# Performance work log

Measured on AMD Instinct MI355X. Metric: run time of the kernel, lower is better.

The kernel has to match this reference:

```python
import jax, jax.numpy as jnp
import numpy as np
from functools import partial

C = 10   # number of regular-repr fields
G = 4    # C4 rotation group order
EPS = 1e-5


def _lift_kernel(w):
    """Lifting (trivial->regular) P4 kernel. w: [C, Cin, k, k] ->
    full kernel [C*G, Cin, k, k] with output channel layout (field, orientation)."""
    ks = [jnp.rot90(w, r, axes=(-2, -1)) for r in range(G)]  # each [C,Cin,k,k]
    k = jnp.stack(ks, axis=1)                                 # [C,G,Cin,k,k]
    return k.reshape(w.shape[0] * G, w.shape[1], w.shape[2], w.shape[3])


def _gconv_kernel(w):
    """Regular->regular P4 kernel. w: [Cout, Cin, G, k, k] (indexed by relative
    input orientation) -> full kernel [Cout*G, Cin*G, k, k].
    K[co*G+r, ci*G+s] = rot90(w[co, ci, (s-r) mod G], r)."""
    Cout, Cin, _, k1, k2 = w.shape
    ks = []
    for r in range(G):
        wr = jnp.roll(w, shift=r, axis=2)             # wr[..., s, :, :] = w[..., (s-r)%G]
        wr = jnp.rot90(wr, r, axes=(-2, -1))          # rotate spatially by r*90deg
        ks.append(wr)
    k = jnp.stack(ks, axis=1)                          # [Cout, G, Cin, G, k, k]
    return k.reshape(Cout * G, Cin * G, k1, k2)


def _conv(x, k, pad):
    return jax.lax.conv_general_dilated(
        x, k, window_strides=(1, 1), padding=pad,
        dimension_numbers=('NCHW', 'OIHW', 'NCHW'))


def _bn_relu(x, gamma, beta):
    """InnerBatchNorm (stats shared over the G orientations of each field) + ReLU."""
    B, CG, H, W = x.shape
    xr = x.reshape(B, C, G, H, W)
    m = xr.mean(axis=(0, 2, 3, 4), keepdims=True)
    v = xr.var(axis=(0, 2, 3, 4), keepdims=True)
    g = gamma[None, :, None, None, None]
    b = beta[None, :, None, None, None]
    y = (xr - m) * jax.lax.rsqrt(v + EPS) * g + b
    return jnp.maximum(y.reshape(B, CG, H, W), 0.0)


def _maxpool2(x):
    return jax.lax.reduce_window(x, -jnp.inf, jax.lax.max,
                                 (1, 1, 2, 2), (1, 1, 2, 2), 'VALID')


def setup_inputs() -> dict:
    key = jax.random.key(0)
    ks = jax.random.split(key, 20)
    B = 1024
    x = jax.random.normal(ks[0], (B, 1, 28, 28), dtype=jnp.float32)
    w1 = jax.random.normal(ks[1], (C, 1, 3, 3), dtype=jnp.float32) * 0.3
    w2 = jax.random.normal(ks[2], (C, C, G, 3, 3), dtype=jnp.float32) * 0.1
    w3 = jax.random.normal(ks[3], (C, C, G, 3, 3), dtype=jnp.float32) * 0.1
    w4 = jax.random.normal(ks[4], (C, C, G, 3, 3), dtype=jnp.float32) * 0.1
    w5 = jax.random.normal(ks[5], (C, C, G, 3, 3), dtype=jnp.float32) * 0.1
    w6 = jax.random.normal(ks[6], (C, C, G, 3, 3), dtype=jnp.float32) * 0.1
    w7 = jax.random.normal(ks[7], (C, C, G, 4, 4), dtype=jnp.float32) * 0.1
    g1 = jnp.ones((C,), jnp.float32) + 0.1 * jax.random.normal(ks[8], (C,))
    b1 = 0.1 * jax.random.normal(ks[9], (C,))
    g2 = jnp.ones((C,), jnp.float32) + 0.1 * jax.random.normal(ks[10], (C,))
    b2 = 0.1 * jax.random.normal(ks[11], (C,))
    gs = jnp.ones((C,), jnp.float32) + 0.1 * jax.random.normal(ks[12], (C,))
    bs = 0.1 * jax.random.normal(ks[13], (C,))
    wfc = jax.random.normal(ks[14], (10, C * 11 * 11), dtype=jnp.float32) * 0.05
    bfc = jnp.zeros((10,), jnp.float32)
    return dict(x=x, w1=w1, w2=w2, w3=w3, w4=w4, w5=w5, w6=w6, w7=w7,
                g1=g1, b1=b1, g2=g2, b2=b2, gs=gs, bs=bs, wfc=wfc, bfc=bfc)


PAD1 = [(1, 1), (1, 1)]
PAD0 = [(0, 0), (0, 0)]


def reference(x, w1, w2, w3, w4, w5, w6, w7, g1, b1, g2, b2, gs, bs, wfc, bfc):
    # block1: lifting P4 conv 3x3 pad1 + InnerBN + ReLU  -> [B, 40, 28, 28]
    h = _bn_relu(_conv(x, _lift_kernel(w1), PAD1), g1, b1)
    # block2: P4 conv + BN + ReLU + 2x2 max pool         -> [B, 40, 14, 14]
    h = _maxpool2(_bn_relu(_conv(h, _gconv_kernel(w2), PAD1), g2, b2))
    # blocks 3-6: P4 conv + shared BN/ReLU               -> [B, 40, 14, 14]
    for w in (w3, w4, w5, w6):
        h = _bn_relu(_conv(h, _gconv_kernel(w), PAD1), gs, bs)
    # block7: P4 conv 4x4 pad0 + shared BN/ReLU          -> [B, 40, 11, 11]
    h = _bn_relu(_conv(h, _gconv_kernel(w7), PAD0), gs, bs)
    # group pooling: max over the G orientations of each field -> [B, 10, 11, 11]
    B = h.shape[0]
    h = h.reshape(B, C, G, 11, 11).max(axis=2)
    # fc
    return h.reshape(B, -1) @ wfc.T + bfc
```

## Files before the change

### kernel.cpp

```cpp
#include <hip/hip_runtime.h>

#define EPSV 1e-5f
#define INV28 (1.f / 3211264.f)
#define INV14 (1.f / 802816.f)
#define INV11 (1.f / 495616.f)

typedef __bf16 v8bf __attribute__((ext_vector_type(8)));
typedef __bf16 v4bf __attribute__((ext_vector_type(4)));
typedef _Float16 v8h __attribute__((ext_vector_type(8)));
typedef _Float16 v4h __attribute__((ext_vector_type(4)));
typedef float v4f __attribute__((ext_vector_type(4)));

__device__ __forceinline__ int rotsrc(int r, int dy, int dx, int K) {
  int sy, sx;
  if (r == 0)      { sy = dy;       sx = dx; }
  else if (r == 1) { sy = dx;       sx = K - 1 - dy; }
  else if (r == 2) { sy = K - 1 - dy; sx = K - 1 - dx; }
  else             { sy = K - 1 - dx; sx = dy; }
  return sy * K + sx;
}

__device__ __forceinline__ float gw_val(const float* __restrict__ w, int oc, int g,
                                        int j, int KS) {
  int tap = g / 5, cig = g % 5, ci = cig * 8 + j;
  int co = oc >> 2, r = oc & 3, cin = ci >> 2, s = ci & 3;
  int srel = (s - r) & 3;
  return w[((co * 10 + cin) * 4 + srel) * (KS * KS) + rotsrc(r, tap / KS, tap % KS, KS)];
}

__device__ __forceinline__ float stat8a(const float* __restrict__ p, int i) {
  float v = 0.f;
#pragma unroll
  for (int c = 0; c < 8; ++c)
    v += __hip_atomic_load(&p[c * 32 + i], __ATOMIC_RELAXED, __HIP_MEMORY_SCOPE_AGENT);
  return v;
}

__global__ void prep_kernel(const float* __restrict__ w1, const float* __restrict__ w2,
                            const float* __restrict__ w3, const float* __restrict__ w4,
                            const float* __restrict__ w5, const float* __restrict__ w6,
                            const float* __restrict__ w7,
                            __bf16* __restrict__ K1b, __bf16* __restrict__ Wb,
                            float* __restrict__ stats) {
  int idx = blockIdx.x * blockDim.x + threadIdx.x;
  if (idx < 1792) { stats[idx] = 0.f; return; }
  idx -= 1792;
  if (idx < 1536) {
    int mt = idx >> 9, l = (idx >> 3) & 63, j = idx & 7;
    int m = l & 15, quad = l >> 4;
    int k = quad * 8 + j, oc = mt * 16 + m;
    float val = 0.f;
    if (k < 9 && oc < 40) {
      int c = oc >> 2, r = oc & 3;
      val = w1[c * 9 + rotsrc(r, k / 3, k % 3, 3)];
    }
    K1b[idx] = (__bf16)val;
    return;
  }
  idx -= 1536;
  if (idx < 92160) {
    int l = idx / 18432, r0 = idx % 18432;
    const float* w = (l == 0) ? w2 : (l == 1) ? w3 : (l == 2) ? w4 : (l == 3) ? w5 : w6;
    int mt = r0 / 6144, r1 = r0 % 6144;
    int c = r1 / 512, r2 = r1 % 512;
    int q = r2 / 128, r3 = r2 % 128;
    int ocl = r3 / 8, j = r3 % 8;
    int oc = mt * 16 + ocl, g = c * 4 + q;
    float val = 0.f;
    if (oc < 40 && g < 45) val = gw_val(w, oc, g, j, 3);
    Wb[idx] = (__bf16)val;
    return;
  }
  idx -= 92160;
  if (idx < 30720) {
    int mt = idx / 10240, r1 = idx % 10240;
    int c = r1 / 512, r2 = r1 % 512;
    int q = r2 / 128, r3 = r2 % 128;
    int ocl = r3 / 8, j = r3 % 8;
    int oc = mt * 16 + ocl, g = c * 4 + q;
    float val = 0.f;
    if (oc < 40) val = gw_val(w7, oc, g, j, 4);
    Wb[92160 + idx] = (__bf16)val;
  }
}

__global__ __launch_bounds__(256) void conv1_stats(
    const float* __restrict__ x, const __bf16* __restrict__ K1b,
    float* __restrict__ stats) {
  __shared__ float ximg[900];
  __shared__ float sstat[20];
  const int tid = threadIdx.x, img = blockIdx.x;
  if (tid < 20) sstat[tid] = 0.f;
  for (int i = tid; i < 900; i += 256) {
    int gy = i / 30 - 1, gx = i % 30 - 1;
    ximg[i] = (gy >= 0 && gy < 28 && gx >= 0 && gx < 28)
                  ? x[img * 784 + gy * 28 + gx] : 0.f;
  }
  __syncthreads();
  const int lane = tid & 63, wv = tid >> 6;
  const int m = lane & 15, quad = lane >> 4;
  v8bf a1[3];
#pragma unroll
  for (int mt = 0; mt < 3; ++mt)
    a1[mt] = *(const v8bf*)(K1b + (mt * 64 + lane) * 8);
  float s[3] = {0.f, 0.f, 0.f}, q[3] = {0.f, 0.f, 0.f};
  for (int st = wv; st < 49; st += 4) {
    const int p = st * 16 + m;
    const int y = p / 28, xx = p % 28;
    v8bf b;
#pragma unroll
    for (int j = 0; j < 8; ++j) {
      const int t = quad * 8 + j;
      float v = 0.f;
      if (t < 9) v = ximg[(y + t / 3) * 30 + xx + t % 3];
      b[j] = (__bf16)v;
    }
#pragma unroll
    for (int mt = 0; mt < 3; ++mt) {
      v4f acc = {0.f, 0.f, 0.f, 0.f};
      acc = __builtin_amdgcn_mfma_f32_16x16x32_bf16(a1[mt], b, acc, 0, 0, 0);
#pragma unroll
      for (int r = 0; r < 4; ++r) { float v = acc[r]; s[mt] += v; q[mt] += v * v; }
    }
  }
#pragma unroll
  for (int mt = 0; mt < 3; ++mt) {
    float sv = s[mt], qv = q[mt];
#pragma unroll
    for (int off = 1; off <= 8; off <<= 1) {
      sv += __shfl_xor(sv, off, 64);
      qv += __shfl_xor(qv, off, 64);
    }
    if (m == 0 && ((mt < 2) || (quad < 2))) {
      atomicAdd(&sstat[mt * 4 + quad], sv);
      atomicAdd(&sstat[10 + mt * 4 + quad], qv);
    }
  }
  __syncthreads();
  if (tid < 20) atomicAdd(&stats[(img & 7) * 32 + tid], sstat[tid]);
}

template<int R>
__global__ __launch_bounds__(256) void conv_band_fused(
    const float* __restrict__ x, const __bf16* __restrict__ K1b,
    const __bf16* __restrict__ Wl, const float* __restrict__ pstats,
    const float* __restrict__ pgamma, const float* __restrict__ pbeta,
    float pinvn, _Float16* __restrict__ T0, float* __restrict__ stats) {
  constexpr int NPIX = R * 28, NSUB = NPIX / 16, NSW = (NSUB + 3) / 4;
  constexpr int SROWS = R + 2, XR = R + 4;
  __shared__ __attribute__((aligned(16))) __bf16 tile[SROWS * 30 * 40];
  __shared__ float xpatch[XR * 32];
  __shared__ float sc[10], sh[10], sstat[20];
  const int tid = threadIdx.x;
  const int lane = tid & 63, wv = tid >> 6;
  const int m = lane & 15, quad = lane >> 4;
  int img, y0;
  if constexpr (R == 8) { img = blockIdx.x / 3; y0 = (blockIdx.x % 3) * 8; }
  else { img = blockIdx.x; y0 = 24; }

  if (tid < 20) sstat[tid] = 0.f;
  if (tid >= 32 && tid < 42) {
    int f = tid - 32;
    float mu = stat8a(pstats, f) * pinvn, q = stat8a(pstats, 10 + f) * pinvn;
    float isd = rsqrtf(q - mu * mu + EPSV);
    float s = pgamma[f] * isd;
    sc[f] = s; sh[f] = pbeta[f] - mu * s;
  }
  for (int i = tid; i < XR * 32; i += 256) {
    int gy = y0 - 2 + i / 32, gx = i % 32 - 2;
    xpatch[i] = (gy >= 0 && gy < 28 && gx >= 0 && gx < 28)
                    ? x[(long)img * 784 + gy * 28 + gx] : 0.f;
  }
  __syncthreads();

  {
    v8bf a1[3];
#pragma unroll
    for (int mt = 0; mt < 3; ++mt)
      a1[mt] = *(const v8bf*)(K1b + (mt * 64 + lane) * 8);
    constexpr int NPIXS = SROWS * 30;
    constexpr int NST = (NPIXS + 15) / 16;
    for (int st = wv; st < NST; st += 4) {
      const int p = st * 16 + m;
      const int pc = p < NPIXS ? p : NPIXS - 1;
      const int iy = pc / 30, ix = pc % 30;
      v8bf b;
#pragma unroll
      for (int j = 0; j < 8; ++j) {
        const int t = quad * 8 + j;
        float v = 0.f;
        if (t < 9) v = xpatch[(iy + t / 3) * 32 + ix + t % 3];
        b[j] = (__bf16)v;
      }
      const int gy = y0 + iy - 1, gx = ix - 1;
      const bool wr = p < NPIXS;
      const bool inb = wr && gy >= 0 && gy < 28 && gx >= 0 && gx < 28;
      __bf16* tb = &tile[pc * 40];
#pragma unroll
      for (int mt = 0; mt < 3; ++mt) {
        v4f acc = {0.f, 0.f, 0.f, 0.f};
        acc = __builtin_amdgcn_mfma_f32_16x16x32_bf16(a1[mt], b, acc, 0, 0, 0);
        if (((mt < 2) || (quad < 2)) && wr) {
          const int f = mt * 4 + quad;
          const float scf = sc[f], shf = sh[f];
          v4bf pk;
#pragma unroll
          for (int r = 0; r < 4; ++r)
            pk[r] = inb ? (__bf16)fmaxf(0.f, fmaf(acc[r], scf, shf)) : (__bf16)0.f;
          *(v4bf*)(tb + mt * 16 + quad * 4) = pk;
        }
      }
    }
  }
  __syncthreads();

  int pbase[NSW], nsv[NSW];
  bool sv[NSW];
#pragma unroll
  for (int s = 0; s < NSW; ++s) {
    int ns = wv + 4 * s;
    sv[s] = ns < NSUB;
    int n = ns * 16 + m;
    n = n < NPIX ? n : NPIX - 1;
    nsv[s] = n;
    pbase[s] = ((n / 28) * 30 + (n % 28)) * 40;
  }
  v4f acc[3][NSW] = {};

  const __bf16* wlane = Wl + (quad * 16 + m) * 8;
  for (int c = 0; c < 12; ++c) {
    int g = 4 * c + quad; g = g > 44 ? 44 : g;
    int tap = g / 5, cig = g - tap * 5;
    int boff = ((tap / 3) * 30 + (tap % 3)) * 40 + cig * 8;
    v8bf bfr[NSW];
#pragma unroll
    for (int s = 0; s < NSW; ++s)
      if (sv[s]) bfr[s] = *(const v8bf*)&tile[pbase[s] + boff];
    v8bf afr[3];
#pragma unroll
    for (int mt = 0; mt < 3; ++mt)
      afr[mt] = *(const v8bf*)(wlane + (mt * 12 + c) * 512);
#pragma unroll
    for (int s = 0; s < NSW; ++s)
      if (sv[s]) {
#pragma unroll
        for (int mt = 0; mt < 3; ++mt)
          acc[mt][s] = __builtin_amdgcn_mfma_f32_16x16x32_bf16(afr[mt], bfr[s],
                                                              acc[mt][s], 0, 0, 0);
      }
  }

#pragma unroll
  for (int mt = 0; mt < 3; ++mt) {
    float svv = 0.f, qvv = 0.f;
#pragma unroll
    for (int s = 0; s < NSW; ++s)
      if (sv[s]) {
#pragma unroll
        for (int r = 0; r < 4; ++r) { float v = acc[mt][s][r]; svv += v; qvv += v * v; }
      }
    const bool ocok = (mt < 2) || (quad < 2);
#pragma unroll
    for (int off = 1; off <= 8; off <<= 1) {
      svv += __shfl_xor(svv, off, 64);
      qvv += __shfl_xor(qvv, off, 64);
    }
    if (m == 0 && ocok) {
      atomicAdd(&sstat[mt * 4 + quad], svv);
      atomicAdd(&sstat[10 + mt * 4 + quad], qvv);
    }
  }

  __syncthreads();
  __bf16* pool = tile;
#pragma unroll
  for (int mt = 0; mt < 3; ++mt) {
    const bool ocok = (mt < 2) || (quad < 2);
    const int oc0 = mt * 16 + quad * 4;
#pragma unroll
    for (int s = 0; s < NSW; ++s)
      if (ocok && sv[s]) {
#pragma unroll
        for (int r = 0; r < 4; ++r)
          pool[(oc0 + r) * NPIX + nsv[s]] = (__bf16)acc[mt][s][r];
      }
  }
  __syncthreads();
  constexpr int PR = R / 2, PCNT = 40 * PR * 14;
  for (int i = tid; i < PCNT; i += 256) {
    int oc = i / (PR * 14), rem = i % (PR * 14);
    int py = rem / 14, px = rem % 14;
    const __bf16* pp = pool + oc * NPIX + py * 56 + px * 2;
    float a = (float)pp[0], b = (float)pp[1], c = (float)pp[28], d = (float)pp[29];
    T0[((long)img * 256 + (y0 / 2 + py + 1) * 16 + (px + 1)) * 40 + oc] =
        (_Float16)fmaxf(fmaxf(a, b), fmaxf(c, d));
  }
  if (tid < 20) atomicAdd(&stats[(img & 7) * 32 + tid], sstat[tid]);
}

__global__ __launch_bounds__(256) void conv_tile(
    const _Float16* __restrict__ Tin, const __bf16* __restrict__ Wl,
    const float* __restrict__ pstats, const float* __restrict__ pg,
    const float* __restrict__ pb, float pinvn,
    _Float16* __restrict__ Tout, float* __restrict__ stG) {
  __shared__ __attribute__((aligned(16))) __bf16 tile[256 * 40];
  __shared__ float sc[10], sh[10], sstat[20];
  const int tid = threadIdx.x, img = blockIdx.x;
  const int lane = tid & 63, wv = tid >> 6;
  const int m = lane & 15, quad = lane >> 4;
  if (tid < 20) sstat[tid] = 0.f;
  if (tid >= 32 && tid < 42) {
    int f = tid - 32;
    float mu = stat8a(pstats, f) * pinvn, q = stat8a(pstats, 10 + f) * pinvn;
    float isd = rsqrtf(q - mu * mu + EPSV);
    float s = pg[f] * isd;
    sc[f] = s; sh[f] = pb[f] - mu * s;
  }
  __syncthreads();
  {
    const int iy = tid >> 4, ix = tid & 15;
    const bool border = (iy == 0) | (iy == 15) | (ix == 0) | (ix == 15);
    const _Float16* src = Tin + ((long)img * 256 + tid) * 40;
    __bf16* dst = &tile[tid * 40];
#pragma unroll
    for (int cg5 = 0; cg5 < 5; ++cg5) {
      v8bf pk;
      if (!border) {
        v8h rv = *(const v8h*)(src + cg5 * 8);
#pragma unroll
        for (int u = 0; u < 8; ++u) {
          const int f = (cg5 * 8 + u) >> 2;
          pk[u] = (__bf16)fmaxf(0.f, fmaf((float)rv[u], sc[f], sh[f]));
        }
      } else {
#pragma unroll
        for (int u = 0; u < 8; ++u) pk[u] = (__bf16)0.f;
      }
      *(v8bf*)(dst + cg5 * 8) = pk;
    }
  }
  __syncthreads();

  int pb3[4], n3[4];
  bool sv3[4], va3[4];
#pragma unroll
  for (int s = 0; s < 4; ++s) {
    int ns = wv + 4 * s;
    sv3[s] = ns < 13;
    int n = ns * 16 + m;
    va3[s] = sv3[s] && (n < 196);
    n = n < 196 ? n : 195;
    n3[s] = n;
    pb3[s] = ((n / 14) * 16 + (n % 14)) * 40;
  }
  const int wofs = (quad * 16 + m) * 8;
  v4f acc[3][4];
#pragma unroll
  for (int mt = 0; mt < 3; ++mt)
#pragma unroll
    for (int s = 0; s < 4; ++s) acc[mt][s] = (v4f){0.f, 0.f, 0.f, 0.f};
  for (int c = 0; c < 12; ++c) {
    int g = 4 * c + quad; g = g > 44 ? 44 : g;
    int tap = g / 5, cig = g - tap * 5;
    int boff = ((tap / 3) * 16 + (tap % 3)) * 40 + cig * 8;
    v8bf bfr[4];
#pragma unroll
    for (int s = 0; s < 4; ++s)
      if (sv3[s]) bfr[s] = *(const v8bf*)&tile[pb3[s] + boff];
    v8bf afr[3];
#pragma unroll
    for (int mt = 0; mt < 3; ++mt)
      afr[mt] = *(const v8bf*)(Wl + wofs + (mt * 12 + c) * 512);
#pragma unroll
    for (int s = 0; s < 4; ++s)
      if (sv3[s]) {
#pragma unroll
        for (int mt = 0; mt < 3; ++mt)
          acc[mt][s] = __builtin_amdgcn_mfma_f32_16x16x32_bf16(afr[mt], bfr[s],
                                                              acc[mt][s], 0, 0, 0);
      }
  }

#pragma unroll
  for (int mt = 0; mt < 3; ++mt) {
    float svv = 0.f, qvv = 0.f;
#pragma unroll
    for (int s = 0; s < 4; ++s)
      if (va3[s]) {
#pragma unroll
        for (int r = 0; r < 4; ++r) { float v = acc[mt][s][r]; svv += v; qvv += v * v; }
      }
    const bool ocok = (mt < 2) || (quad < 2);
#pragma unroll
    for (int off = 1; off <= 8; off <<= 1) {
      svv += __shfl_xor(svv, off, 64);
      qvv += __shfl_xor(qvv, off, 64);
    }
    if (m == 0 && ocok) {
      atomicAdd(&sstat[mt * 4 + quad], svv);
      atomicAdd(&sstat[10 + mt * 4 + quad], qvv);
    }
  }
  __syncthreads();
  if (tid < 20) atomicAdd(&stG[(img & 7) * 32 + tid], sstat[tid]);

#pragma unroll
  for (int mt = 0; mt < 3; ++mt) {
    const bool ocok = (mt < 2) || (quad < 2);
    if (!ocok) continue;
#pragma unroll
    for (int s = 0; s < 4; ++s)
      if (va3[s]) {
        v4h pk;
#pragma unroll
        for (int r = 0; r < 4; ++r) pk[r] = (_Float16)acc[mt][s][r];
        const int n = n3[s];
        *(v4h*)(Tout + ((long)img * 256 + (n / 14 + 1) * 16 + (n % 14 + 1)) * 40
                + mt * 16 + quad * 4) = pk;
      }
  }
}

__global__ __launch_bounds__(256) void conv7_tile(
    const _Float16* __restrict__ Tin, const __bf16* __restrict__ Wl,
    const float* __restrict__ pstats, const float* __restrict__ pg,
    const float* __restrict__ pb,
    _Float16* __restrict__ T7, float* __restrict__ stG) {
  __shared__ __attribute__((aligned(16))) __bf16 tile[256 * 40];
  __shared__ float sc[10], sh[10], sstat[20];
  const int tid = threadIdx.x, img = blockIdx.x;
  const int lane = tid & 63, wv = tid >> 6;
  const int m = lane & 15, quad = lane >> 4;
  if (tid < 20) sstat[tid] = 0.f;
  if (tid >= 32 && tid < 42) {
    int f = tid - 32;
    float mu = stat8a(pstats, f) * INV14, q = stat8a(pstats, 10 + f) * INV14;
    float isd = rsqrtf(q - mu * mu + EPSV);
    float s = pg[f] * isd;
    sc[f] = s; sh[f] = pb[f] - mu * s;
  }
  __syncthreads();
  {
    const int iy = tid >> 4, ix = tid & 15;
    const bool border = (iy == 0) | (iy == 15) | (ix == 0) | (ix == 15);
    const _Float16* src = Tin + ((long)img * 256 + tid) * 40;
    __bf16* dst = &tile[tid * 40];
#pragma unroll
    for (int cg5 = 0; cg5 < 5; ++cg5) {
      v8bf pk;
      if (!border) {
        v8h rv = *(const v8h*)(src + cg5 * 8);
#pragma unroll
        for (int u = 0; u < 8; ++u) {
          const int f = (cg5 * 8 + u) >> 2;
          pk[u] = (__bf16)fmaxf(0.f, fmaf((float)rv[u], sc[f], sh[f]));
        }
      } else {
#pragma unroll
        for (int u = 0; u < 8; ++u) pk[u] = (__bf16)0.f;
      }
      *(v8bf*)(dst + cg5 * 8) = pk;
    }
  }
  __syncthreads();

  int pb7[2], n7[2];
  bool va7[2];
#pragma unroll
  for (int s = 0; s < 2; ++s) {
    int ns = wv + 4 * s;
    int n = ns * 16 + m;
    va7[s] = n < 121;
    n = n < 121 ? n : 120;
    n7[s] = n;
    pb7[s] = ((n / 11 + 1) * 16 + (n % 11 + 1)) * 40;
  }
  const int wofs = (quad * 16 + m) * 8;
  v4f acc[3][2];
#pragma unroll
  for (int mt = 0; mt < 3; ++mt)
#pragma unroll
    for (int s = 0; s < 2; ++s) acc[mt][s] = (v4f){0.f, 0.f, 0.f, 0.f};
  for (int c = 0; c < 20; ++c) {
    int g = 4 * c + quad;
    int tap = g / 5, cig = g - tap * 5;
    int boff = ((tap >> 2) * 16 + (tap & 3)) * 40 + cig * 8;
    v8bf bfr[2];
#pragma unroll
    for (int s = 0; s < 2; ++s) bfr[s] = *(const v8bf*)&tile[pb7[s] + boff];
    v8bf afr[3];
#pragma unroll
    for (int mt = 0; mt < 3; ++mt)
      afr[mt] = *(const v8bf*)(Wl + wofs + (mt * 20 + c) * 512);
#pragma unroll
    for (int s = 0; s < 2; ++s)
#pragma unroll
      for (int mt = 0; mt < 3; ++mt)
        acc[mt][s] = __builtin_amdgcn_mfma_f32_16x16x32_bf16(afr[mt], bfr[s],
                                                            acc[mt][s], 0, 0, 0);
  }

#pragma unroll
  for (int mt = 0; mt < 3; ++mt) {
    float svv = 0.f, qvv = 0.f;
#pragma unroll
    for (int s = 0; s < 2; ++s)
      if (va7[s]) {
#pragma unroll
        for (int r = 0; r < 4; ++r) { float v = acc[mt][s][r]; svv += v; qvv += v * v; }
      }
    const bool ocok = (mt < 2) || (quad < 2);
#pragma unroll
    for (int off = 1; off <= 8; off <<= 1) {
      svv += __shfl_xor(svv, off, 64);
      qvv += __shfl_xor(qvv, off, 64);
    }
    if (m == 0 && ocok) {
      atomicAdd(&sstat[mt * 4 + quad], svv);
      atomicAdd(&sstat[10 + mt * 4 + quad], qvv);
    }
  }
  __syncthreads();
  if (tid < 20) atomicAdd(&stG[(img & 7) * 32 + tid], sstat[tid]);

#pragma unroll
  for (int mt = 0; mt < 3; ++mt) {
    const bool ocok = (mt < 2) || (quad < 2);
    if (!ocok) continue;
#pragma unroll
    for (int s = 0; s < 2; ++s)
      if (va7[s]) {
        v4h pk;
#pragma unroll
        for (int r = 0; r < 4; ++r) pk[r] = (_Float16)acc[mt][s][r];
        *(v4h*)(T7 + ((long)img * 121 + n7[s]) * 40 + mt * 16 + quad * 4) = pk;
      }
  }
}

__global__ __launch_bounds__(256) void head_kernel(
    const _Float16* __restrict__ T7, const float* __restrict__ stats7,
    const float* __restrict__ gs, const float* __restrict__ bs,
    const float* __restrict__ wfc, const float* __restrict__ bfc,
    float* __restrict__ out) {
  __shared__ float sc[10], sh[10];
  __shared__ float mbuf[1210];
  __shared__ float red[40];
  const int tid = threadIdx.x, img = blockIdx.x;
  if (tid < 10) {
    float mu = stat8a(stats7, tid) * INV11, q = stat8a(stats7, 10 + tid) * INV11;
    float isd = rsqrtf(q - mu * mu + EPSV);
    float s = gs[tid] * isd;
    sc[tid] = s;
    sh[tid] = bs[tid] - mu * s;
  }
  __syncthreads();
  for (int p = tid; p < 121; p += 256) {
    const _Float16* rp = T7 + ((long)img * 121 + p) * 40;
#pragma unroll
    for (int cg5 = 0; cg5 < 5; ++cg5) {
      v8h v = *(const v8h*)(rp + cg5 * 8);
#pragma unroll
      for (int fh = 0; fh < 2; ++fh) {
        const int f = cg5 * 2 + fh;
        float mx = fmaf((float)v[fh * 4], sc[f], sh[f]);
#pragma unroll
        for (int r = 1; r < 4; ++r)
          mx = fmaxf(mx, fmaf((float)v[fh * 4 + r], sc[f], sh[f]));
        mbuf[f * 121 + p] = fmaxf(0.f, mx);
      }
    }
  }
  __syncthreads();
  const int wv = tid >> 6;
  for (int k = 0; k < 10; ++k) {
    float p = 0.f;
    for (int j = tid; j < 1210; j += 256) p = fmaf(mbuf[j], wfc[k * 1210 + j], p);
#pragma unroll
    for (int off = 32; off > 0; off >>= 1) p += __shfl_xor(p, off, 64);
    if ((tid & 63) == 0) red[k * 4 + wv] = p;
  }
  __syncthreads();
  if (tid < 10)
    out[img * 10 + tid] = bfc[tid] + red[tid * 4] + red[tid * 4 + 1] +
                          red[tid * 4 + 2] + red[tid * 4 + 3];
}

extern "C" void kernel_launch(void* const* d_in, const int* in_sizes, int n_in,
                              void* d_out, int out_size, void* d_ws, size_t ws_size,
                              hipStream_t stream) {
  const float* x   = (const float*)d_in[0];
  const float* w1  = (const float*)d_in[1];
  const float* w2  = (const float*)d_in[2];
  const float* w3  = (const float*)d_in[3];
  const float* w4  = (const float*)d_in[4];
  const float* w5  = (const float*)d_in[5];
  const float* w6  = (const float*)d_in[6];
  const float* w7  = (const float*)d_in[7];
  const float* g1  = (const float*)d_in[8];
  const float* b1  = (const float*)d_in[9];
  const float* g2  = (const float*)d_in[10];
  const float* b2  = (const float*)d_in[11];
  const float* gs  = (const float*)d_in[12];
  const float* bs  = (const float*)d_in[13];
  const float* wfc = (const float*)d_in[14];
  const float* bfc = (const float*)d_in[15];

  float* ws = (float*)d_ws;
  float* stats = ws;
  __bf16* K1b  = (__bf16*)(ws + 1792);
  __bf16* Wb   = (__bf16*)(ws + 2560);
  _Float16* T0 = (_Float16*)(ws + 64000);
  _Float16* T1 = (_Float16*)(ws + 5306880L);
  _Float16* T7 = (_Float16*)(ws + 10549760L);

  prep_kernel<<<493, 256, 0, stream>>>(w1, w2, w3, w4, w5, w6, w7, K1b, Wb, stats);
  conv1_stats<<<1024, 256, 0, stream>>>(x, K1b, stats);
  conv_band_fused<8><<<3072, 256, 0, stream>>>(x, K1b, Wb, stats, g1, b1, INV28,
                                               T0, stats + 256);
  conv_band_fused<4><<<1024, 256, 0, stream>>>(x, K1b, Wb, stats, g1, b1, INV28,
                                               T0, stats + 256);
  conv_tile<<<1024, 256, 0, stream>>>(T0, Wb + 18432, stats + 256, g2, b2, INV28,
                                      T1, stats + 512);
  conv_tile<<<1024, 256, 0, stream>>>(T1, Wb + 36864, stats + 512, gs, bs, INV14,
                                      T0, stats + 768);
  conv_tile<<<1024, 256, 0, stream>>>(T0, Wb + 55296, stats + 768, gs, bs, INV14,
                                      T1, stats + 1024);
  conv_tile<<<1024, 256, 0, stream>>>(T1, Wb + 73728, stats + 1024, gs, bs, INV14,
                                      T0, stats + 1280);
  conv7_tile<<<1024, 256, 0, stream>>>(T0, Wb + 92160, stats + 1280, gs, bs,
                                       T7, stats + 1536);
  head_kernel<<<1024, 256, 0, stream>>>(T7, stats + 1536, gs, bs, wfc, bfc,
                                        (float*)d_out);
}
```

Before: 290.9 us.

## Switch MFMA path to fp16, fuse band kernels, pool via lane shuffles

Moves weights and tiles from bf16 to fp16 and uses the f16 MFMA variant. This removes bf16 conversions when loading fp16 activations, and the BN+ReLU prologue is now done with packed half2 math. The two band kernels (8-row and 4-row) are merged into one launch of 4096 blocks. The second conv's pixel order is remapped so each 2x2 pool window falls in 4 adjacent lanes, which lets max-pooling run with cross-lane shuffles instead of an LDS round trip and two syncthreads. Doing BN scale/shift in fp16 and using fp16 range may cost some precision or risk overflow.

```diff
diff --git a/kernel.cpp b/kernel.cpp
--- a/kernel.cpp
+++ b/kernel.cpp
@@ -5,11 +5,19 @@
 #define INV14 (1.f / 802816.f)
 #define INV11 (1.f / 495616.f)
 
-typedef __bf16 v8bf __attribute__((ext_vector_type(8)));
-typedef __bf16 v4bf __attribute__((ext_vector_type(4)));
 typedef _Float16 v8h __attribute__((ext_vector_type(8)));
 typedef _Float16 v4h __attribute__((ext_vector_type(4)));
+typedef _Float16 v2h __attribute__((ext_vector_type(2)));
 typedef float v4f __attribute__((ext_vector_type(4)));
+
+__device__ __forceinline__ int h2i(v2h v) { union { v2h h; int i; } u; u.h = v; return u.i; }
+__device__ __forceinline__ v2h i2h(int i) { union { v2h h; int i; } u; u.i = i; return u.h; }
+__device__ __forceinline__ int pmax2(int a, int b) {
+  v2h x = i2h(a), y = i2h(b), r;
+  r[0] = x[0] > y[0] ? x[0] : y[0];
+  r[1] = x[1] > y[1] ? x[1] : y[1];
+  return h2i(r);
+}
 
 __device__ __forceinline__ int rotsrc(int r, int dy, int dx, int K) {
   int sy, sx;
@@ -40,7 +48,7 @@
                             const float* __restrict__ w3, const float* __restrict__ w4,
                             const float* __restrict__ w5, const float* __restrict__ w6,
                             const float* __restrict__ w7,
-                            __bf16* __restrict__ K1b, __bf16* __restrict__ Wb,
+                            _Float16* __restrict__ K1h, _Float16* __restrict__ Wh,
                             float* __restrict__ stats) {
   int idx = blockIdx.x * blockDim.x + threadIdx.x;
   if (idx < 1792) { stats[idx] = 0.f; return; }
@@ -54,7 +62,7 @@
       int c = oc >> 2, r = oc & 3;
       val = w1[c * 9 + rotsrc(r, k / 3, k % 3, 3)];
     }
-    K1b[idx] = (__bf16)val;
+    K1h[idx] = (_Float16)val;
     return;
   }
   idx -= 1536;
@@ -68,7 +76,7 @@
     int oc = mt * 16 + ocl, g = c * 4 + q;
     float val = 0.f;
     if (oc < 40 && g < 45) val = gw_val(w, oc, g, j, 3);
-    Wb[idx] = (__bf16)val;
+    Wh[idx] = (_Float16)val;
     return;
   }
   idx -= 92160;
@@ -80,12 +88,12 @@
     int oc = mt * 16 + ocl, g = c * 4 + q;
     float val = 0.f;
     if (oc < 40) val = gw_val(w7, oc, g, j, 4);
-    Wb[92160 + idx] = (__bf16)val;
+    Wh[92160 + idx] = (_Float16)val;
   }
 }
 
 __global__ __launch_bounds__(256) void conv1_stats(
-    const float* __restrict__ x, const __bf16* __restrict__ K1b,
+    const float* __restrict__ x, const _Float16* __restrict__ K1h,
     float* __restrict__ stats) {
   __shared__ float ximg[900];
   __shared__ float sstat[20];
@@ -99,26 +107,26 @@
   __syncthreads();
   const int lane = tid & 63, wv = tid >> 6;
   const int m = lane & 15, quad = lane >> 4;
-  v8bf a1[3];
+  v8h a1[3];
 #pragma unroll
   for (int mt = 0; mt < 3; ++mt)
-    a1[mt] = *(const v8bf*)(K1b + (mt * 64 + lane) * 8);
+    a1[mt] = *(const v8h*)(K1h + (mt * 64 + lane) * 8);
   float s[3] = {0.f, 0.f, 0.f}, q[3] = {0.f, 0.f, 0.f};
   for (int st = wv; st < 49; st += 4) {
     const int p = st * 16 + m;
     const int y = p / 28, xx = p % 28;
-    v8bf b;
+    v8h b;
 #pragma unroll
     for (int j = 0; j < 8; ++j) {
       const int t = quad * 8 + j;
       float v = 0.f;
       if (t < 9) v = ximg[(y + t / 3) * 30 + xx + t % 3];
-      b[j] = (__bf16)v;
+      b[j] = (_Float16)v;
     }
 #pragma unroll
     for (int mt = 0; mt < 3; ++mt) {
       v4f acc = {0.f, 0.f, 0.f, 0.f};
-      acc = __builtin_amdgcn_mfma_f32_16x16x32_bf16(a1[mt], b, acc, 0, 0, 0);
+      acc = __builtin_amdgcn_mfma_f32_16x16x32_f16(a1[mt], b, acc, 0, 0, 0);
 #pragma unroll
       for (int r = 0; r < 4; ++r) { float v = acc[r]; s[mt] += v; q[mt] += v * v; }
     }
@@ -141,31 +149,19 @@
 }
 
 template<int R>
-__global__ __launch_bounds__(256) void conv_band_fused(
-    const float* __restrict__ x, const __bf16* __restrict__ K1b,
-    const __bf16* __restrict__ Wl, const float* __restrict__ pstats,
-    const float* __restrict__ pgamma, const float* __restrict__ pbeta,
-    float pinvn, _Float16* __restrict__ T0, float* __restrict__ stats) {
+__device__ __forceinline__ void band_impl(
+    const int img, const int y0,
+    const float* __restrict__ x, const _Float16* __restrict__ K1h,
+    const _Float16* __restrict__ Wl,
+    float* __restrict__ xpatch, _Float16* __restrict__ tile,
+    const float* __restrict__ sc, const float* __restrict__ sh,
+    float* __restrict__ sstat, _Float16* __restrict__ T0) {
   constexpr int NPIX = R * 28, NSUB = NPIX / 16, NSW = (NSUB + 3) / 4;
   constexpr int SROWS = R + 2, XR = R + 4;
-  __shared__ __attribute__((aligned(16))) __bf16 tile[SROWS * 30 * 40];
-  __shared__ float xpatch[XR * 32];
-  __shared__ float sc[10], sh[10], sstat[20];
   const int tid = threadIdx.x;
   const int lane = tid & 63, wv = tid >> 6;
   const int m = lane & 15, quad = lane >> 4;
-  int img, y0;
-  if constexpr (R == 8) { img = blockIdx.x / 3; y0 = (blockIdx.x % 3) * 8; }
-  else { img = blockIdx.x; y0 = 24; }
-
-  if (tid < 20) sstat[tid] = 0.f;
-  if (tid >= 32 && tid < 42) {
-    int f = tid - 32;
-    float mu = stat8a(pstats, f) * pinvn, q = stat8a(pstats, 10 + f) * pinvn;
-    float isd = rsqrtf(q - mu * mu + EPSV);
-    float s = pgamma[f] * isd;
-    sc[f] = s; sh[f] = pbeta[f] - mu * s;
-  }
+
   for (int i = tid; i < XR * 32; i += 256) {
     int gy = y0 - 2 + i / 32, gx = i % 32 - 2;
     xpatch[i] = (gy >= 0 && gy < 28 && gx >= 0 && gx < 28)
@@ -174,79 +170,79 @@
   __syncthreads();
 
   {
-    v8bf a1[3];
+    v8h a1[3];
 #pragma unroll
     for (int mt = 0; mt < 3; ++mt)
-      a1[mt] = *(const v8bf*)(K1b + (mt * 64 + lane) * 8);
+      a1[mt] = *(const v8h*)(K1h + (mt * 64 + lane) * 8);
     constexpr int NPIXS = SROWS * 30;
     constexpr int NST = (NPIXS + 15) / 16;
     for (int st = wv; st < NST; st += 4) {
       const int p = st * 16 + m;
       const int pc = p < NPIXS ? p : NPIXS - 1;
       const int iy = pc / 30, ix = pc % 30;
-      v8bf b;
+      v8h b;
 #pragma unroll
       for (int j = 0; j < 8; ++j) {
         const int t = quad * 8 + j;
         float v = 0.f;
         if (t < 9) v = xpatch[(iy + t / 3) * 32 + ix + t % 3];
-        b[j] = (__bf16)v;
+        b[j] = (_Float16)v;
       }
       const int gy = y0 + iy - 1, gx = ix - 1;
       const bool wr = p < NPIXS;
       const bool inb = wr && gy >= 0 && gy < 28 && gx >= 0 && gx < 28;
-      __bf16* tb = &tile[pc * 40];
+      _Float16* tb = &tile[pc * 40];
 #pragma unroll
       for (int mt = 0; mt < 3; ++mt) {
-        v4f acc = {0.f, 0.f, 0.f, 0.f};
-        acc = __builtin_amdgcn_mfma_f32_16x16x32_bf16(a1[mt], b, acc, 0, 0, 0);
+        v4f a = {0.f, 0.f, 0.f, 0.f};
+        a = __builtin_amdgcn_mfma_f32_16x16x32_f16(a1[mt], b, a, 0, 0, 0);
         if (((mt < 2) || (quad < 2)) && wr) {
           const int f = mt * 4 + quad;
           const float scf = sc[f], shf = sh[f];
-          v4bf pk;
+          v4h pk;
 #pragma unroll
           for (int r = 0; r < 4; ++r)
-            pk[r] = inb ? (__bf16)fmaxf(0.f, fmaf(acc[r], scf, shf)) : (__bf16)0.f;
-          *(v4bf*)(tb + mt * 16 + quad * 4) = pk;
+            pk[r] = inb ? (_Float16)fmaxf(0.f, fmaf(a[r], scf, shf)) : (_Float16)0.f;
+          *(v4h*)(tb + mt * 16 + quad * 4) = pk;
         }
       }
     }
   }
   __syncthreads();
 
-  int pbase[NSW], nsv[NSW];
+  int pbase[NSW];
   bool sv[NSW];
 #pragma unroll
   for (int s = 0; s < NSW; ++s) {
     int ns = wv + 4 * s;
     sv[s] = ns < NSUB;
-    int n = ns * 16 + m;
-    n = n < NPIX ? n : NPIX - 1;
-    nsv[s] = n;
-    pbase[s] = ((n / 28) * 30 + (n % 28)) * 40;
+    int i = (sv[s] ? ns : 0) * 16 + m;
+    int q = i >> 2, c2 = i & 3;
+    int yy = 2 * (q / 14) + (c2 >> 1), xx = 2 * (q % 14) + (c2 & 1);
+    pbase[s] = (yy * 30 + xx) * 40;
   }
   v4f acc[3][NSW] = {};
 
-  const __bf16* wlane = Wl + (quad * 16 + m) * 8;
+  const _Float16* wlane = Wl + (quad * 16 + m) * 8;
   for (int c = 0; c < 12; ++c) {
     int g = 4 * c + quad; g = g > 44 ? 44 : g;
     int tap = g / 5, cig = g - tap * 5;
     int boff = ((tap / 3) * 30 + (tap % 3)) * 40 + cig * 8;
-    v8bf bfr[NSW];
+    v8h bfr[NSW];
 #pragma unroll
     for (int s = 0; s < NSW; ++s)
-      if (sv[s]) bfr[s] = *(const v8bf*)&tile[pbase[s] + boff];
-    v8bf afr[3];
+      if (sv[s]) bfr[s] = *(const v8h*)&tile[pbase[s] + boff];
+    v8h afr[3];
 #pragma unroll
     for (int mt = 0; mt < 3; ++mt)
-      afr[mt] = *(const v8bf*)(wlane + (mt * 12 + c) * 512);
+      afr[mt] = *(const v8h*)(wlane + (mt * 12 + c) * 512);
 #pragma unroll
     for (int s = 0; s < NSW; ++s)
       if (sv[s]) {
 #pragma unroll
         for (int mt = 0; mt < 3; ++mt)
-          acc[mt][s] = __builtin_amdgcn_mfma_f32_16x16x32_bf16(afr[mt], bfr[s],
-                                                              acc[mt][s], 0, 0, 0);
+          acc[mt][s] = __builtin_amdgcn_mfma_f32_16x16x32_f16(afr[mt], bfr[s],
+                                                             acc[mt][s], 0, 0, 0);
       }
   }
 
@@ -271,40 +267,72 @@
     }
   }
 
-  __syncthreads();
-  __bf16* pool = tile;
-#pragma unroll
-  for (int mt = 0; mt < 3; ++mt) {
-    const bool ocok = (mt < 2) || (quad < 2);
-    const int oc0 = mt * 16 + quad * 4;
-#pragma unroll
-    for (int s = 0; s < NSW; ++s)
-      if (ocok && sv[s]) {
-#pragma unroll
-        for (int r = 0; r < 4; ++r)
-          pool[(oc0 + r) * NPIX + nsv[s]] = (__bf16)acc[mt][s][r];
-      }
-  }
-  __syncthreads();
-  constexpr int PR = R / 2, PCNT = 40 * PR * 14;
-  for (int i = tid; i < PCNT; i += 256) {
-    int oc = i / (PR * 14), rem = i % (PR * 14);
-    int py = rem / 14, px = rem % 14;
-    const __bf16* pp = pool + oc * NPIX + py * 56 + px * 2;
-    float a = (float)pp[0], b = (float)pp[1], c = (float)pp[28], d = (float)pp[29];
-    T0[((long)img * 256 + (y0 / 2 + py + 1) * 16 + (px + 1)) * 40 + oc] =
-        (_Float16)fmaxf(fmaxf(a, b), fmaxf(c, d));
-  }
+#pragma unroll
+  for (int s = 0; s < NSW; ++s) {
+    if (!sv[s]) continue;
+    const int ns = wv + 4 * s;
+    const int q = ns * 4 + (m >> 2);
+    const int tb4 = (img * 256 + (y0 / 2 + q / 14 + 1) * 16 + (q % 14 + 1)) * 40;
+#pragma unroll
+    for (int mt = 0; mt < 3; ++mt) {
+      const bool ocok = (mt < 2) || (quad < 2);
+      if (!ocok) continue;
+      v2h w0, w1;
+      w0[0] = (_Float16)acc[mt][s][0]; w0[1] = (_Float16)acc[mt][s][1];
+      w1[0] = (_Float16)acc[mt][s][2]; w1[1] = (_Float16)acc[mt][s][3];
+      int a0 = h2i(w0), a1 = h2i(w1);
+      a0 = pmax2(a0, __shfl_xor(a0, 1, 64));
+      a0 = pmax2(a0, __shfl_xor(a0, 2, 64));
+      a1 = pmax2(a1, __shfl_xor(a1, 1, 64));
+      a1 = pmax2(a1, __shfl_xor(a1, 2, 64));
+      if ((m & 3) == 0) {
+        v2h r0 = i2h(a0), r1 = i2h(a1);
+        v4h o;
+        o[0] = r0[0]; o[1] = r0[1]; o[2] = r1[0]; o[3] = r1[1];
+        *(v4h*)(T0 + (long)tb4 + mt * 16 + quad * 4) = o;
+      }
+    }
+  }
+}
+
+__global__ __launch_bounds__(256) void conv_band_all(
+    const float* __restrict__ x, const _Float16* __restrict__ K1h,
+    const _Float16* __restrict__ Wl, const float* __restrict__ pstats,
+    const float* __restrict__ pgamma, const float* __restrict__ pbeta,
+    _Float16* __restrict__ T0, float* __restrict__ stats) {
+  __shared__ __attribute__((aligned(16))) _Float16 tile[10 * 30 * 40];
+  __shared__ float xpatch[12 * 32];
+  __shared__ float sc[10], sh[10], sstat[20];
+  const int tid = threadIdx.x;
+  if (tid < 20) sstat[tid] = 0.f;
+  if (tid >= 32 && tid < 42) {
+    int f = tid - 32;
+    float mu = stat8a(pstats, f) * INV28, q = stat8a(pstats, 10 + f) * INV28;
+    float isd = rsqrtf(q - mu * mu + EPSV);
+    float s = pgamma[f] * isd;
+    sc[f] = s; sh[f] = pbeta[f] - mu * s;
+  }
+  const int bid = blockIdx.x;
+  int img;
+  if (bid < 3072) {
+    img = bid / 3;
+    band_impl<8>(img, (bid % 3) * 8, x, K1h, Wl, xpatch, tile, sc, sh, sstat, T0);
+  } else {
+    img = bid - 3072;
+    band_impl<4>(img, 24, x, K1h, Wl, xpatch, tile, sc, sh, sstat, T0);
+  }
+  __syncthreads();
   if (tid < 20) atomicAdd(&stats[(img & 7) * 32 + tid], sstat[tid]);
 }
 
 __global__ __launch_bounds__(256) void conv_tile(
-    const _Float16* __restrict__ Tin, const __bf16* __restrict__ Wl,
+    const _Float16* __restrict__ Tin, const _Float16* __restrict__ Wl,
     const float* __restrict__ pstats, const float* __restrict__ pg,
     const float* __restrict__ pb, float pinvn,
     _Float16* __restrict__ Tout, float* __restrict__ stG) {
-  __shared__ __attribute__((aligned(16))) __bf16 tile[256 * 40];
-  __shared__ float sc[10], sh[10], sstat[20];
+  __shared__ __attribute__((aligned(16))) _Float16 tile[256 * 40];
+  __shared__ v2h scH[10], shH[10];
+  __shared__ float sstat[20];
   const int tid = threadIdx.x, img = blockIdx.x;
   const int lane = tid & 63, wv = tid >> 6;
   const int m = lane & 15, quad = lane >> 4;
@@ -314,29 +342,40 @@
     float mu = stat8a(pstats, f) * pinvn, q = stat8a(pstats, 10 + f) * pinvn;
     float isd = rsqrtf(q - mu * mu + EPSV);
     float s = pg[f] * isd;
-    sc[f] = s; sh[f] = pb[f] - mu * s;
+    _Float16 sH = (_Float16)s, hH = (_Float16)(pb[f] - mu * s);
+    v2h t0, t1;
+    t0[0] = sH; t0[1] = sH; t1[0] = hH; t1[1] = hH;
+    scH[f] = t0; shH[f] = t1;
   }
   __syncthreads();
   {
     const int iy = tid >> 4, ix = tid & 15;
     const bool border = (iy == 0) | (iy == 15) | (ix == 0) | (ix == 15);
     const _Float16* src = Tin + ((long)img * 256 + tid) * 40;
-    __bf16* dst = &tile[tid * 40];
-#pragma unroll
-    for (int cg5 = 0; cg5 < 5; ++cg5) {
-      v8bf pk;
-      if (!border) {
+    _Float16* dst = &tile[tid * 40];
+    if (!border) {
+#pragma unroll
+      for (int cg5 = 0; cg5 < 5; ++cg5) {
         v8h rv = *(const v8h*)(src + cg5 * 8);
-#pragma unroll
-        for (int u = 0; u < 8; ++u) {
-          const int f = (cg5 * 8 + u) >> 2;
-          pk[u] = (__bf16)fmaxf(0.f, fmaf((float)rv[u], sc[f], sh[f]));
+        v2h* r2 = (v2h*)&rv;
+        v8h pk; v2h* p2 = (v2h*)&pk;
+#pragma unroll
+        for (int pr = 0; pr < 4; ++pr) {
+          const int f = cg5 * 2 + (pr >> 1);
+          v2h t = r2[pr] * scH[f] + shH[f];
+          v2h o;
+          o[0] = t[0] > (_Float16)0.f ? t[0] : (_Float16)0.f;
+          o[1] = t[1] > (_Float16)0.f ? t[1] : (_Float16)0.f;
+          p2[pr] = o;
         }
-      } else {
-#pragma unroll
-        for (int u = 0; u < 8; ++u) pk[u] = (__bf16)0.f;
-      }
-      *(v8bf*)(dst + cg5 * 8) = pk;
+        *(v8h*)(dst + cg5 * 8) = pk;
+      }
+    } else {
+      v8h z;
+#pragma unroll
+      for (int u = 0; u < 8; ++u) z[u] = (_Float16)0.f;
+#pragma unroll
+      for (int cg5 = 0; cg5 < 5; ++cg5) *(v8h*)(dst + cg5 * 8) = z;
     }
   }
   __syncthreads();
@@ -363,21 +402,21 @@
     int g = 4 * c + quad; g = g > 44 ? 44 : g;
     int tap = g / 5, cig = g - tap * 5;
     int boff = ((tap / 3) * 16 + (tap % 3)) * 40 + cig * 8;
-    v8bf bfr[4];
+    v8h bfr[4];
 #pragma unroll
     for (int s = 0; s < 4; ++s)
-      if (sv3[s]) bfr[s] = *(const v8bf*)&tile[pb3[s] + boff];
-    v8bf afr[3];
+      if (sv3[s]) bfr[s] = *(const v8h*)&tile[pb3[s] + boff];
+    v8h afr[3];
 #pragma unroll
     for (int mt = 0; mt < 3; ++mt)
-      afr[mt] = *(const v8bf*)(Wl + wofs + (mt * 12 + c) * 512);
+      afr[mt] = *(const v8h*)(Wl + wofs + (mt * 12 + c) * 512);
 #pragma unroll
     for (int s = 0; s < 4; ++s)
       if (sv3[s]) {
 #pragma unroll
         for (int mt = 0; mt < 3; ++mt)
-          acc[mt][s] = __builtin_amdgcn_mfma_f32_16x16x32_bf16(afr[mt], bfr[s],
-                                                              acc[mt][s], 0, 0, 0);
+          acc[mt][s] = __builtin_amdgcn_mfma_f32_16x16x32_f16(afr[mt], bfr[s],
+                                                             acc[mt][s], 0, 0, 0);
       }
   }
 
@@ -422,12 +461,13 @@
 }
 
 __global__ __launch_bounds__(256) void conv7_tile(
-    const _Float16* __restrict__ Tin, const __bf16* __restrict__ Wl,
+    const _Float16* __restrict__ Tin, const _Float16* __restrict__ Wl,
     const float* __restrict__ pstats, const float* __restrict__ pg,
     const float* __restrict__ pb,
     _Float16* __restrict__ T7, float* __restrict__ stG) {
-  __shared__ __attribute__((aligned(16))) __bf16 tile[256 * 40];
-  __shared__ float sc[10], sh[10], sstat[20];
+  __shared__ __attribute__((aligned(16))) _Float16 tile[256 * 40];
+  __shared__ v2h scH[10], shH[10];
+  __shared__ float sstat[20];
   const int tid = threadIdx.x, img = blockIdx.x;
   const int lane = tid & 63, wv = tid >> 6;
   const int m = lane & 15, quad = lane >> 4;
@@ -437,29 +477,40 @@
     float mu = stat8a(pstats, f) * INV14, q = stat8a(pstats, 10 + f) * INV14;
     float isd = rsqrtf(q - mu * mu + EPSV);
     float s = pg[f] * isd;
-    sc[f] = s; sh[f] = pb[f] - mu * s;
+    _Float16 sH = (_Float16)s, hH = (_Float16)(pb[f] - mu * s);
+    v2h t0, t1;
+    t0[0] = sH; t0[1] = sH; t1[0] = hH; t1[1] = hH;
+    scH[f] = t0; shH[f] = t1;
   }
   __syncthreads();
   {
     const int iy = tid >> 4, ix = tid & 15;
     const bool border = (iy == 0) | (iy == 15) | (ix == 0) | (ix == 15);
     const _Float16* src = Tin + ((long)img * 256 + tid) * 40;
-    __bf16* dst = &tile[tid * 40];
-#pragma unroll
-    for (int cg5 = 0; cg5 < 5; ++cg5) {
-      v8bf pk;
-      if (!border) {
+    _Float16* dst = &tile[tid * 40];
+    if (!border) {
+#pragma unroll
+      for (int cg5 = 0; cg5 < 5; ++cg5) {
         v8h rv = *(const v8h*)(src + cg5 * 8);
-#pragma unroll
-        for (int u = 0; u < 8; ++u) {
-          const int f = (cg5 * 8 + u) >> 2;
-          pk[u] = (__bf16)fmaxf(0.f, fmaf((float)rv[u], sc[f], sh[f]));
+        v2h* r2 = (v2h*)&rv;
+        v8h pk; v2h* p2 = (v2h*)&pk;
+#pragma unroll
+        for (int pr = 0; pr < 4; ++pr) {
+          const int f = cg5 * 2 + (pr >> 1);
+          v2h t = r2[pr] * scH[f] + shH[f];
+          v2h o;
+          o[0] = t[0] > (_Float16)0.f ? t[0] : (_Float16)0.f;
+          o[1] = t[1] > (_Float16)0.f ? t[1] : (_Float16)0.f;
+          p2[pr] = o;
         }
-      } else {
-#pragma unroll
-        for (int u = 0; u < 8; ++u) pk[u] = (__bf16)0.f;
-      }
-      *(v8bf*)(dst + cg5 * 8) = pk;
+        *(v8h*)(dst + cg5 * 8) = pk;
+      }
+    } else {
+      v8h z;
+#pragma unroll
+      for (int u = 0; u < 8; ++u) z[u] = (_Float16)0.f;
+#pragma unroll
+      for (int cg5 = 0; cg5 < 5; ++cg5) *(v8h*)(dst + cg5 * 8) = z;
     }
   }
   __syncthreads();
@@ -485,19 +536,19 @@
     int g = 4 * c + quad;
     int tap = g / 5, cig = g - tap * 5;
     int boff = ((tap >> 2) * 16 + (tap & 3)) * 40 + cig * 8;
-    v8bf bfr[2];
-#pragma unroll
-    for (int s = 0; s < 2; ++s) bfr[s] = *(const v8bf*)&tile[pb7[s] + boff];
-    v8bf afr[3];
+    v8h bfr[2];
+#pragma unroll
+    for (int s = 0; s < 2; ++s) bfr[s] = *(const v8h*)&tile[pb7[s] + boff];
+    v8h afr[3];
 #pragma unroll
     for (int mt = 0; mt < 3; ++mt)
-      afr[mt] = *(const v8bf*)(Wl + wofs + (mt * 20 + c) * 512);
+      afr[mt] = *(const v8h*)(Wl + wofs + (mt * 20 + c) * 512);
 #pragma unroll
     for (int s = 0; s < 2; ++s)
 #pragma unroll
       for (int mt = 0; mt < 3; ++mt)
-        acc[mt][s] = __builtin_amdgcn_mfma_f32_16x16x32_bf16(afr[mt], bfr[s],
-                                                            acc[mt][s], 0, 0, 0);
+        acc[mt][s] = __builtin_amdgcn_mfma_f32_16x16x32_f16(afr[mt], bfr[s],
+                                                           acc[mt][s], 0, 0, 0);
   }
 
 #pragma unroll
@@ -607,28 +658,26 @@
   const float* bfc = (const float*)d_in[15];
 
   float* ws = (float*)d_ws;
-  float* stats = ws;
-  __bf16* K1b  = (__bf16*)(ws + 1792);
-  __bf16* Wb   = (__bf16*)(ws + 2560);
-  _Float16* T0 = (_Float16*)(ws + 64000);
-  _Float16* T1 = (_Float16*)(ws + 5306880L);
-  _Float16* T7 = (_Float16*)(ws + 10549760L);
-
-  prep_kernel<<<493, 256, 0, stream>>>(w1, w2, w3, w4, w5, w6, w7, K1b, Wb, stats);
-  conv1_stats<<<1024, 256, 0, stream>>>(x, K1b, stats);
-  conv_band_fused<8><<<3072, 256, 0, stream>>>(x, K1b, Wb, stats, g1, b1, INV28,
-                                               T0, stats + 256);
-  conv_band_fused<4><<<1024, 256, 0, stream>>>(x, K1b, Wb, stats, g1, b1, INV28,
-                                               T0, stats + 256);
-  conv_tile<<<1024, 256, 0, stream>>>(T0, Wb + 18432, stats + 256, g2, b2, INV28,
+  float* stats  = ws;
+  _Float16* K1h = (_Float16*)(ws + 1792);
+  _Float16* Wh  = (_Float16*)(ws + 2560);
+  _Float16* T0  = (_Float16*)(ws + 64000);
+  _Float16* T1  = (_Float16*)(ws + 5306880L);
+  _Float16* T7  = (_Float16*)(ws + 10549760L);
+
+  prep_kernel<<<493, 256, 0, stream>>>(w1, w2, w3, w4, w5, w6, w7, K1h, Wh, stats);
+  conv1_stats<<<1024, 256, 0, stream>>>(x, K1h, stats);
+  conv_band_all<<<4096, 256, 0, stream>>>(x, K1h, Wh, stats, g1, b1, T0,
+                                          stats + 256);
+  conv_tile<<<1024, 256, 0, stream>>>(T0, Wh + 18432, stats + 256, g2, b2, INV28,
                                       T1, stats + 512);
-  conv_tile<<<1024, 256, 0, stream>>>(T1, Wb + 36864, stats + 512, gs, bs, INV14,
+  conv_tile<<<1024, 256, 0, stream>>>(T1, Wh + 36864, stats + 512, gs, bs, INV14,
                                       T0, stats + 768);
-  conv_tile<<<1024, 256, 0, stream>>>(T0, Wb + 55296, stats + 768, gs, bs, INV14,
+  conv_tile<<<1024, 256, 0, stream>>>(T0, Wh + 55296, stats + 768, gs, bs, INV14,
                                       T1, stats + 1024);
-  conv_tile<<<1024, 256, 0, stream>>>(T1, Wb + 73728, stats + 1024, gs, bs, INV14,
+  conv_tile<<<1024, 256, 0, stream>>>(T1, Wh + 73728, stats + 1024, gs, bs, INV14,
                                       T0, stats + 1280);
-  conv7_tile<<<1024, 256, 0, stream>>>(T0, Wb + 92160, stats + 1280, gs, bs,
+  conv7_tile<<<1024, 256, 0, stream>>>(T0, Wh + 92160, stats + 1280, gs, bs,
                                        T7, stats + 1536);
   head_kernel<<<1024, 256, 0, stream>>>(T7, stats + 1536, gs, bs, wfc, bfc,
                                         (float*)d_out);
```

New measurement: 265.3 us. 8.8% less time.
